# Kernel optimization log

Measured on AMD Instinct MI355X. Metric: run time of the kernel, lower is better.

## Reference

```python
import jax, jax.numpy as jnp
import numpy as np

B, L, D, H = 2, 2048, 1024, 16
HD = D // H
SCALE = HD ** (-0.5)


def setup_inputs() -> dict:
    key = jax.random.key(0)
    ks = jax.random.split(key, 12)
    mk = lambda k, shape: (0.02 * jax.random.normal(k, shape, dtype=jnp.float32))
    return {
        "x_real": jax.random.normal(ks[0], (B, L, D), dtype=jnp.float32),
        "x_imag": jax.random.normal(ks[1], (B, L, D), dtype=jnp.float32),
        "wq_r": mk(ks[2], (D, D)),
        "wq_i": mk(ks[3], (D, D)),
        "wk_r": mk(ks[4], (D, D)),
        "wk_i": mk(ks[5], (D, D)),
        "wv_r": mk(ks[6], (D, D)),
        "wv_i": mk(ks[7], (D, D)),
        "wo_r": mk(ks[8], (D, D)),
        "wo_i": mk(ks[9], (D, D)),
        "bo_r": jnp.zeros((D,), dtype=jnp.float32),
        "bo_i": jnp.zeros((D,), dtype=jnp.float32),
    }


def _clinear(xr, xi, wr, wi):
    # (a+bi)(c+di): real = a@Wr^T - b@Wi^T ; imag = a@Wi^T + b@Wr^T
    r = xr @ wr.T - xi @ wi.T
    i = xr @ wi.T + xi @ wr.T
    return r, i


def _heads(t):
    # [B,L,D] -> [B,H,L,hd]
    return t.reshape(B, L, H, HD).transpose(0, 2, 1, 3)


def reference(x_real, x_imag, wq_r, wq_i, wk_r, wk_i, wv_r, wv_i, wo_r, wo_i, bo_r, bo_i):
    Qr, Qi = _clinear(x_real, x_imag, wq_r, wq_i)
    Kr, Ki = _clinear(x_real, x_imag, wk_r, wk_i)
    Vr, Vi = _clinear(x_real, x_imag, wv_r, wv_i)
    Qr, Qi, Kr, Ki, Vr, Vi = map(_heads, (Qr, Qi, Kr, Ki, Vr, Vi))

    # real part of complex dot product: Re(Q)Re(K)^T + Im(Q)Im(K)^T
    scores = (jnp.einsum("bhqd,bhkd->bhqk", Qr, Kr)
              + jnp.einsum("bhqd,bhkd->bhqk", Qi, Ki)) * SCALE
    causal = jnp.tril(jnp.ones((L, L), dtype=bool))
    scores = jnp.where(causal, scores, -jnp.inf)
    w = jax.nn.softmax(scores, axis=-1)

    out_r = jnp.einsum("bhqk,bhkd->bhqd", w, Vr)
    out_i = jnp.einsum("bhqk,bhkd->bhqd", w, Vi)
    merge = lambda t: t.transpose(0, 2, 1, 3).reshape(B, L, D)
    out_r, out_i = merge(out_r), merge(out_i)

    yr, yi = _clinear(out_r, out_i, wo_r, wo_i)
    return yr + bo_r, yi + bo_i
```

## Files before the change

kernel.cpp:

```cpp
#include <hip/hip_runtime.h>
#include <hip/hip_bf16.h>


using f32x4  = __attribute__((ext_vector_type(4))) float;
using short8 = __attribute__((ext_vector_type(8))) short;
using bf16_t = __hip_bfloat16;

#define AS1 __attribute__((address_space(1)))
#define AS3 __attribute__((address_space(3)))

__device__ __forceinline__ void gload_lds16(const bf16_t* g, bf16_t* l) {
  __builtin_amdgcn_global_load_lds((const AS1 unsigned int*)g, (AS3 unsigned int*)l, 16, 0, 0);
}

__device__ __forceinline__ unsigned short bfbits(float f) {
  union { bf16_t h; unsigned short u; } c; c.h = __float2bfloat16(f); return c.u;
}

__global__ void pack_x_k(const float* __restrict__ xr, const float* __restrict__ xi,
                         bf16_t* __restrict__ out) {
  const int total4 = 4096 * 2048 / 4;
  for (int idx = blockIdx.x * blockDim.x + threadIdx.x; idx < total4;
       idx += gridDim.x * blockDim.x) {
    int m = idx >> 9, k = (idx & 511) * 4;
    const float* src = (k < 1024) ? (xr + (size_t)m * 1024 + k)
                                  : (xi + (size_t)m * 1024 + (k - 1024));
    float4 v = *(const float4*)src;
    unsigned int lo = (unsigned)bfbits(v.x) | ((unsigned)bfbits(v.y) << 16);
    unsigned int hi = (unsigned)bfbits(v.z) | ((unsigned)bfbits(v.w) << 16);
    *(uint2*)(out + (size_t)idx * 4) = make_uint2(lo, hi);
  }
}

__global__ void pack_wqkv_k(const float* __restrict__ wqr, const float* __restrict__ wqi,
                            const float* __restrict__ wkr, const float* __restrict__ wki,
                            const float* __restrict__ wvr, const float* __restrict__ wvi,
                            bf16_t* __restrict__ out) {
  const int total4 = 6144 * 2048 / 4;
  for (int idx = blockIdx.x * blockDim.x + threadIdx.x; idx < total4;
       idx += gridDim.x * blockDim.x) {
    int row = idx >> 9, k = (idx & 511) * 4;
    int sec = row >> 10, r1 = row & 1023;
    bool lowk = (k < 1024);
    int kk = lowk ? k : (k - 1024);
    const float* base = wqr; float sg = 1.f;
    switch (sec) {
      case 0: base = lowk ? wqr : wqi; sg = lowk ? 1.f : -1.f; break;
      case 1: base = lowk ? wqi : wqr; break;
      case 2: base = lowk ? wkr : wki; sg = lowk ? 1.f : -1.f; break;
      case 3: base = lowk ? wki : wkr; break;
      case 4: base = lowk ? wvr : wvi; sg = lowk ? 1.f : -1.f; break;
      case 5: base = lowk ? wvi : wvr; break;
    }
    float4 v = *(const float4*)(base + (size_t)r1 * 1024 + kk);
    unsigned int lo = (unsigned)bfbits(v.x * sg) | ((unsigned)bfbits(v.y * sg) << 16);
    unsigned int hi = (unsigned)bfbits(v.z * sg) | ((unsigned)bfbits(v.w * sg) << 16);
    *(uint2*)(out + (size_t)idx * 4) = make_uint2(lo, hi);
  }
}

__global__ void pack_wo_k(const float* __restrict__ wor, const float* __restrict__ woi,
                          bf16_t* __restrict__ out) {
  const int total4 = 2048 * 2048 / 4;
  for (int idx = blockIdx.x * blockDim.x + threadIdx.x; idx < total4;
       idx += gridDim.x * blockDim.x) {
    int row = idx >> 9, k = (idx & 511) * 4;
    int sec = row >> 10, r1 = row & 1023;
    bool lowk = (k < 1024);
    int kk = lowk ? k : (k - 1024);
    const float* base; float sg = 1.f;
    if (sec == 0) { base = lowk ? wor : woi; sg = lowk ? 1.f : -1.f; }
    else          { base = lowk ? woi : wor; }
    float4 v = *(const float4*)(base + (size_t)r1 * 1024 + kk);
    unsigned int lo = (unsigned)bfbits(v.x * sg) | ((unsigned)bfbits(v.y * sg) << 16);
    unsigned int hi = (unsigned)bfbits(v.z * sg) | ((unsigned)bfbits(v.w * sg) << 16);
    *(uint2*)(out + (size_t)idx * 4) = make_uint2(lo, hi);
  }
}

__device__ __forceinline__ void gemm_core(const bf16_t* __restrict__ A,
                                          const bf16_t* __restrict__ W,
                                          int m0, int n0, f32x4 (&acc)[4][4]) {
  __shared__ __align__(16) bf16_t sA[128 * 64];
  __shared__ __align__(16) bf16_t sB[128 * 64];
  const int tid = threadIdx.x;
  const int lane = tid & 63, w = tid >> 6;
  const int wr = w >> 1, wc = w & 1;
  const int quad = lane >> 4, m16 = lane & 15;
  const int srow = w * 32 + (lane >> 3);
  const int gcol = (((lane & 7) ^ (lane >> 3)) * 8);
  const int swz7 = m16 & 7;
  for (int k0 = 0; k0 < 2048; k0 += 64) {
    __syncthreads();
#pragma unroll
    for (int i = 0; i < 4; ++i) {
      gload_lds16(A + (size_t)(m0 + srow + i * 8) * 2048 + k0 + gcol,
                  sA + (size_t)(w * 32 + i * 8) * 64 + lane * 8);
      gload_lds16(W + (size_t)(n0 + srow + i * 8) * 2048 + k0 + gcol,
                  sB + (size_t)(w * 32 + i * 8) * 64 + lane * 8);
    }
    __syncthreads();
#pragma unroll
    for (int kk = 0; kk < 2; ++kk) {
      short8 af[4], bf[4];
#pragma unroll
      for (int i = 0; i < 4; ++i)
        af[i] = *(const short8*)(sA + (wr * 64 + i * 16 + m16) * 64 +
                                 ((kk * 4 + quad) ^ swz7) * 8);
#pragma unroll
      for (int j = 0; j < 4; ++j)
        bf[j] = *(const short8*)(sB + (wc * 64 + j * 16 + m16) * 64 +
                                 ((kk * 4 + quad) ^ swz7) * 8);
#pragma unroll
      for (int i = 0; i < 4; ++i)
#pragma unroll
        for (int j = 0; j < 4; ++j)
          acc[i][j] = __builtin_amdgcn_mfma_f32_16x16x32_bf16(af[i], bf[j], acc[i][j], 0, 0, 0);
    }
  }
}

__global__ __launch_bounds__(256) void gemm_qkv_k(const bf16_t* __restrict__ A,
                                                  const bf16_t* __restrict__ W,
                                                  bf16_t* __restrict__ qk,
                                                  bf16_t* __restrict__ vt) {
  f32x4 acc[4][4] = {};
  const int m0 = blockIdx.x * 128, n0 = blockIdx.y * 128;
  gemm_core(A, W, m0, n0, acc);
  const int lane = threadIdx.x & 63, w = threadIdx.x >> 6;
  const int wr = w >> 1, wc = w & 1, quad = lane >> 4, m16 = lane & 15;
#pragma unroll
  for (int i = 0; i < 4; ++i) {
    const int rowb = m0 + wr * 64 + i * 16 + quad * 4;
#pragma unroll
    for (int j = 0; j < 4; ++j) {
      const int col = n0 + wc * 64 + j * 16 + m16;
      if (col < 4096) {
        const float sc = (col < 2048) ? 0.125f : 1.f;
#pragma unroll
        for (int r = 0; r < 4; ++r)
          qk[(size_t)(rowb + r) * 4096 + col] = __float2bfloat16(acc[i][j][r] * sc);
      } else {
        const int vcol = col - 4096;
        const int ri = vcol >> 10, dfeat = vcol & 1023;
        const int b = rowb >> 11, seq = rowb & 2047;
        const size_t vrow = (size_t)(b * 2048 + (dfeat >> 6) * 128 + ri * 64 + (dfeat & 63));
        unsigned int lo = (unsigned)bfbits(acc[i][j][0]) | ((unsigned)bfbits(acc[i][j][1]) << 16);
        unsigned int hi = (unsigned)bfbits(acc[i][j][2]) | ((unsigned)bfbits(acc[i][j][3]) << 16);
        *(uint2*)(vt + vrow * 2048 + seq) = make_uint2(lo, hi);
      }
    }
  }
}

__global__ __launch_bounds__(256) void gemm_out_k(const bf16_t* __restrict__ A,
                                                  const bf16_t* __restrict__ W,
                                                  const float* __restrict__ bor,
                                                  const float* __restrict__ boi,
                                                  float* __restrict__ out) {
  f32x4 acc[4][4] = {};
  const int m0 = blockIdx.x * 128, n0 = blockIdx.y * 128;
  gemm_core(A, W, m0, n0, acc);
  const int lane = threadIdx.x & 63, w = threadIdx.x >> 6;
  const int wr = w >> 1, wc = w & 1, quad = lane >> 4, m16 = lane & 15;
#pragma unroll
  for (int i = 0; i < 4; ++i) {
    const int rowb = m0 + wr * 64 + i * 16 + quad * 4;
#pragma unroll
    for (int j = 0; j < 4; ++j) {
      const int col = n0 + wc * 64 + j * 16 + m16;
      float bias; float* op;
      if (col < 1024) { bias = bor[col]; op = out + col; }
      else            { bias = boi[col - 1024]; op = out + 4194304 + (col - 1024); }
#pragma unroll
      for (int r = 0; r < 4; ++r)
        op[(size_t)(rowb + r) * 1024] = acc[i][j][r] + bias;
    }
  }
}

__global__ __launch_bounds__(512, 4) void attn_k(const bf16_t* __restrict__ qk,
                                                 const bf16_t* __restrict__ vt,
                                                 bf16_t* __restrict__ acat) {
  __shared__ __align__(16) bf16_t sK[64 * 128];
  __shared__ __align__(16) bf16_t sV[144 * 64];
  __shared__ __align__(16) bf16_t sP[8][16 * 72];
  const int tid = threadIdx.x, lane = tid & 63, w = tid >> 6;
  const int wq = w & 3, sub = w >> 2;
  const int quad = lane >> 4, m16 = lane & 15;
  const int x = blockIdx.x, bh = blockIdx.y, b = bh >> 4, h = bh & 15;
  const size_t qkrow0 = (size_t)b * 2048;
  const int qA = x * 64, qB = (31 - x) * 64;
  const int nT = 32 - x;
  const int swz7 = m16 & 7;
  const int qbase = (sub ? qB : qA) + wq * 16;

  if (tid < 256) {
    const int rr = tid >> 4, cb = (tid & 15) * 4;
    const bf16_t v = __float2bfloat16(rr == 0 ? 1.f : 0.f);
#pragma unroll
    for (int i = 0; i < 4; ++i) sV[(128 + rr) * 64 + cb + i] = v;
  }

  short8 qf[4];
  {
    const bf16_t* qa = qk + (qkrow0 + qbase + m16) * 4096;
#pragma unroll
    for (int kk = 0; kk < 4; ++kk) {
      const int col = (kk >> 1) * 1024 + h * 64 + (kk & 1) * 32 + quad * 8;
      qf[kk] = *(const short8*)(qa + col);
    }
  }
  f32x4 o[9];
#pragma unroll
  for (int j = 0; j < 9; ++j) o[j] = (f32x4){0.f, 0.f, 0.f, 0.f};

  const int qrow = qbase + quad * 4;

  const int kl4 = lane >> 4, kl15 = lane & 15;
  const int vl3 = lane >> 3;
  const int vg7 = ((lane & 7) ^ vl3) * 8;

  for (int t = 0; t < nT; ++t) {
    const int k0 = t * 64;
    __syncthreads();
#pragma unroll
    for (int i = 0; i < 2; ++i) {
      const int row = w * 8 + i * 4 + kl4;
      const int g = kl15 ^ (row & 7);
      const int col = 2048 + (g >> 3) * 1024 + h * 64 + (g & 7) * 8;
      gload_lds16(qk + (qkrow0 + k0 + row) * 4096 + col,
                  sK + (size_t)(w * 8 + i * 4) * 128 + lane * 8);
    }
#pragma unroll
    for (int i = 0; i < 2; ++i) {
      const int row = w * 16 + i * 8 + vl3;
      gload_lds16(vt + ((size_t)bh * 128 + row) * 2048 + k0 + vg7,
                  sV + (size_t)(w * 16 + i * 8) * 64 + lane * 8);
    }
    __syncthreads();

    const bool act = sub ? true : (t <= x);
    if (act) {
      const bool dg = sub ? (t == nT - 1) : (t == x);

      f32x4 sv[4];
#pragma unroll
      for (int jt = 0; jt < 4; ++jt) {
        f32x4 a = (f32x4){0.f, 0.f, 0.f, 0.f};
#pragma unroll
        for (int kk = 0; kk < 4; ++kk) {
          short8 kf = *(const short8*)(sK + (jt * 16 + m16) * 128 +
                                       ((kk * 4 + quad) ^ swz7) * 8);
          a = __builtin_amdgcn_mfma_f32_16x16x32_bf16(qf[kk], kf, a, 0, 0, 0);
        }
        sv[jt] = a;
      }

      bf16_t* pw = sP[w];
#pragma unroll
      for (int jt = 0; jt < 4; ++jt)
#pragma unroll
        for (int r = 0; r < 4; ++r) {
          float s = sv[jt][r];
          if (dg && (k0 + jt * 16 + m16 > qrow + r)) s = -1e30f;
          pw[(quad * 4 + r) * 72 + jt * 16 + m16] = __float2bfloat16(__expf(s));
        }
      asm volatile("s_waitcnt lgkmcnt(0)" ::: "memory");

#pragma unroll
      for (int kc = 0; kc < 2; ++kc) {
        short8 p = *(const short8*)(pw + m16 * 72 + kc * 32 + quad * 8);
#pragma unroll
        for (int j = 0; j < 9; ++j) {
          short8 vf = *(const short8*)(sV + (j * 16 + m16) * 64 +
                                       ((kc * 4 + quad) ^ swz7) * 8);
          o[j] = __builtin_amdgcn_mfma_f32_16x16x32_bf16(p, vf, o[j], 0, 0, 0);
        }
      }
    }
  }

  float inv[4];
#pragma unroll
  for (int r = 0; r < 4; ++r)
    inv[r] = 1.f / __shfl(o[8][r], lane & 48);
#pragma unroll
  for (int j = 0; j < 8; ++j) {
    const int d = j * 16 + m16;
    const int col = (d < 64) ? (h * 64 + d) : (1024 + h * 64 + (d - 64));
#pragma unroll
    for (int r = 0; r < 4; ++r)
      acat[((size_t)b * 2048 + qrow + r) * 2048 + col] = __float2bfloat16(o[j][r] * inv[r]);
  }
}

extern "C" void kernel_launch(void* const* d_in, const int* in_sizes, int n_in,
                              void* d_out, int out_size, void* d_ws, size_t ws_size,
                              hipStream_t stream) {
  const float* xr  = (const float*)d_in[0];
  const float* xi  = (const float*)d_in[1];
  const float* wqr = (const float*)d_in[2];
  const float* wqi = (const float*)d_in[3];
  const float* wkr = (const float*)d_in[4];
  const float* wki = (const float*)d_in[5];
  const float* wvr = (const float*)d_in[6];
  const float* wvi = (const float*)d_in[7];
  const float* wor = (const float*)d_in[8];
  const float* woi = (const float*)d_in[9];
  const float* bor = (const float*)d_in[10];
  const float* boi = (const float*)d_in[11];
  float* out = (float*)d_out;

  char* ws = (char*)d_ws;
  bf16_t* Xcat = (bf16_t*)(ws);
  bf16_t* Wqkv = (bf16_t*)(ws + 16777216ull);
  bf16_t* QKb  = (bf16_t*)(ws + 41943040ull);
  bf16_t* Vt   = (bf16_t*)(ws + 75497472ull);
  bf16_t* Acat = (bf16_t*)(ws + 92274688ull);
  bf16_t* Wo   = (bf16_t*)(ws + 109051904ull);

  pack_x_k<<<2048, 256, 0, stream>>>(xr, xi, Xcat);
  pack_wqkv_k<<<2048, 256, 0, stream>>>(wqr, wqi, wkr, wki, wvr, wvi, Wqkv);
  pack_wo_k<<<1024, 256, 0, stream>>>(wor, woi, Wo);
  gemm_qkv_k<<<dim3(32, 48), 256, 0, stream>>>(Xcat, Wqkv, QKb, Vt);
  attn_k<<<dim3(16, 32), 512, 0, stream>>>(QKb, Vt, Acat);
  gemm_out_k<<<dim3(32, 16), 256, 0, stream>>>(Acat, Wo, bor, boi, out);
}
```

Measured before the change: 362.0 us.

## Rewrite QKV GEMM with 256x256 tiles and interleaved double-buffered LDS prefetch

Replaces the shared 128x128 gemm_core path for the QKV projection with a dedicated 512-thread kernel that computes 256x256 tiles. Global-to-LDS loads for the next K slices are issued between MFMA groups, with explicit vmcnt waits, barriers and setprio. The larger tile is meant to cut global and LDS traffic per FLOP, and the interleaving is meant to hide load latency behind compute. In exchange it uses 128KB of LDS per block and more accumulator registers, and the grid shrinks to 384 blocks, which may limit occupancy.

```diff
diff --git a/kernel.cpp b/kernel.cpp
--- a/kernel.cpp
+++ b/kernel.cpp
@@ -120,33 +120,104 @@
   }
 }
 
-__global__ __launch_bounds__(256) void gemm_qkv_k(const bf16_t* __restrict__ A,
-                                                  const bf16_t* __restrict__ W,
-                                                  bf16_t* __restrict__ qk,
-                                                  bf16_t* __restrict__ vt) {
-  f32x4 acc[4][4] = {};
-  const int m0 = blockIdx.x * 128, n0 = blockIdx.y * 128;
-  gemm_core(A, W, m0, n0, acc);
-  const int lane = threadIdx.x & 63, w = threadIdx.x >> 6;
-  const int wr = w >> 1, wc = w & 1, quad = lane >> 4, m16 = lane & 15;
-#pragma unroll
-  for (int i = 0; i < 4; ++i) {
-    const int rowb = m0 + wr * 64 + i * 16 + quad * 4;
-#pragma unroll
-    for (int j = 0; j < 4; ++j) {
-      const int col = n0 + wc * 64 + j * 16 + m16;
+__global__ __launch_bounds__(512, 2) void gemm_qkv_k(const bf16_t* __restrict__ A,
+                                                     const bf16_t* __restrict__ W,
+                                                     bf16_t* __restrict__ qk,
+                                                     bf16_t* __restrict__ vt) {
+  __shared__ __align__(16) bf16_t sA[2][256 * 64];
+  __shared__ __align__(16) bf16_t sB[2][256 * 64];
+  const int tid = threadIdx.x, lane = tid & 63, w = tid >> 6;
+  const int wm = w >> 2, wn = w & 3;
+  const int quad = lane >> 4, m16 = lane & 15;
+  const int swz7 = m16 & 7;
+  const int m0 = blockIdx.x * 256, n0 = blockIdx.y * 256;
+  const int NT = 32;
+
+  const int srow = w * 16 + (lane >> 3);
+  const int gcol = (((lane & 7) ^ (lane >> 3)) * 8);
+
+  f32x4 acc[8][4] = {};
+
+  auto stageA = [&](int buf, int half, int k0) {
+#pragma unroll
+    for (int i = 0; i < 2; ++i)
+      gload_lds16(A + (size_t)(m0 + half * 128 + srow + i * 8) * 2048 + k0 + gcol,
+                  &sA[buf][(size_t)(half * 128 + w * 16 + i * 8) * 64] + lane * 8);
+  };
+  auto stageB = [&](int buf, int half, int k0) {
+#pragma unroll
+    for (int i = 0; i < 2; ++i)
+      gload_lds16(W + (size_t)(n0 + half * 128 + srow + i * 8) * 2048 + k0 + gcol,
+                  &sB[buf][(size_t)(half * 128 + w * 16 + i * 8) * 64] + lane * 8);
+  };
+
+  stageA(0, 0, 0); stageA(0, 1, 0);
+  stageB(0, 0, 0); stageB(0, 1, 0);
+  stageA(1, 0, 64); stageA(1, 1, 64);
+  asm volatile("s_waitcnt vmcnt(4)" ::: "memory");
+  __builtin_amdgcn_s_barrier();
+
+  for (int t = 0; t < NT; ++t) {
+    const int p = t & 1, q = p ^ 1;
+    const bf16_t* sAp = sA[p];
+    const bf16_t* sBp = sB[p];
+    short8 af[8][2];
+#pragma unroll
+    for (int nf = 0; nf < 4; ++nf) {
+      if (nf == 0) {
+#pragma unroll
+        for (int mf = 0; mf < 8; ++mf)
+#pragma unroll
+          for (int kk = 0; kk < 2; ++kk)
+            af[mf][kk] = *(const short8*)(sAp + (wm * 128 + mf * 16 + m16) * 64 +
+                                          ((kk * 4 + quad) ^ swz7) * 8);
+      }
+      short8 bf[2];
+#pragma unroll
+      for (int kk = 0; kk < 2; ++kk)
+        bf[kk] = *(const short8*)(sBp + (wn * 64 + nf * 16 + m16) * 64 +
+                                  ((kk * 4 + quad) ^ swz7) * 8);
+      if (nf == 0)      { if (t + 1 < NT) stageB(q, 0, (t + 1) * 64); }
+      else if (nf == 1) { if (t + 1 < NT) stageB(q, 1, (t + 1) * 64); }
+      else if (nf == 2) { if (t + 2 < NT) stageA(p, 0, (t + 2) * 64); }
+      else              { if (t + 2 < NT) stageA(p, 1, (t + 2) * 64); }
+      asm volatile("" ::: "memory");
+      __builtin_amdgcn_s_barrier();
+      __builtin_amdgcn_s_setprio(1);
+#pragma unroll
+      for (int mf = 0; mf < 8; ++mf)
+#pragma unroll
+        for (int kk = 0; kk < 2; ++kk)
+          acc[mf][nf] = __builtin_amdgcn_mfma_f32_16x16x32_bf16(af[mf][kk], bf[kk],
+                                                                acc[mf][nf], 0, 0, 0);
+      __builtin_amdgcn_s_setprio(0);
+      asm volatile("" ::: "memory");
+      if (nf == 3) {
+        if (t == NT - 2)      asm volatile("s_waitcnt vmcnt(0)" ::: "memory");
+        else if (t < NT - 2)  asm volatile("s_waitcnt vmcnt(4)" ::: "memory");
+      }
+      __builtin_amdgcn_s_barrier();
+    }
+  }
+
+#pragma unroll
+  for (int mf = 0; mf < 8; ++mf) {
+    const int rowb = m0 + wm * 128 + mf * 16 + quad * 4;
+#pragma unroll
+    for (int nf = 0; nf < 4; ++nf) {
+      const int col = n0 + wn * 64 + nf * 16 + m16;
       if (col < 4096) {
         const float sc = (col < 2048) ? 0.125f : 1.f;
 #pragma unroll
         for (int r = 0; r < 4; ++r)
-          qk[(size_t)(rowb + r) * 4096 + col] = __float2bfloat16(acc[i][j][r] * sc);
+          qk[(size_t)(rowb + r) * 4096 + col] = __float2bfloat16(acc[mf][nf][r] * sc);
       } else {
         const int vcol = col - 4096;
         const int ri = vcol >> 10, dfeat = vcol & 1023;
         const int b = rowb >> 11, seq = rowb & 2047;
         const size_t vrow = (size_t)(b * 2048 + (dfeat >> 6) * 128 + ri * 64 + (dfeat & 63));
-        unsigned int lo = (unsigned)bfbits(acc[i][j][0]) | ((unsigned)bfbits(acc[i][j][1]) << 16);
-        unsigned int hi = (unsigned)bfbits(acc[i][j][2]) | ((unsigned)bfbits(acc[i][j][3]) << 16);
+        unsigned int lo = (unsigned)bfbits(acc[mf][nf][0]) | ((unsigned)bfbits(acc[mf][nf][1]) << 16);
+        unsigned int hi = (unsigned)bfbits(acc[mf][nf][2]) | ((unsigned)bfbits(acc[mf][nf][3]) << 16);
         *(uint2*)(vt + vrow * 2048 + seq) = make_uint2(lo, hi);
       }
     }
@@ -323,7 +394,7 @@
   pack_x_k<<<2048, 256, 0, stream>>>(xr, xi, Xcat);
   pack_wqkv_k<<<2048, 256, 0, stream>>>(wqr, wqi, wkr, wki, wvr, wvi, Wqkv);
   pack_wo_k<<<1024, 256, 0, stream>>>(wor, woi, Wo);
-  gemm_qkv_k<<<dim3(32, 48), 256, 0, stream>>>(Xcat, Wqkv, QKb, Vt);
+  gemm_qkv_k<<<dim3(16, 24), 512, 0, stream>>>(Xcat, Wqkv, QKb, Vt);
   attn_k<<<dim3(16, 32), 512, 0, stream>>>(QKb, Vt, Acat);
   gemm_out_k<<<dim3(32, 16), 256, 0, stream>>>(Acat, Wo, bor, boi, out);
 }
```

Measured after the change: 383.4 us. 1.06x slower.
